# Performance work log

Measured on AMD Instinct MI355X. Metric: run time of the kernel, lower is better.

Reference implementation:

```python
import jax, jax.numpy as jnp
import numpy as np

ICM2IFS = 2.99792458e-05
KB = 0.6950389


def _forward(T, Er, cortim, dt, psi0, Hfull, W1, b1, W2, b2, W3, b3, W4, b4,
             save_interval, remat=False):
    # Faithful vectorized translation of MLNISE.forward with T_correction='ML',
    # explicitTemp='None', saveCoherence=False, saveU=False. The original
    # nested (ii, jj) Python loops are fully independent across (ii, jj), so
    # they are vectorized into one [B, N, N] pass per timestep.
    B, Tp1, N, _ = Hfull.shape
    kBT = T * KB                                             # [B]
    factor = (1j * 2.0 * np.pi * ICM2IFS) * dt.astype(jnp.complex64)  # [B]
    E0, C0 = jnp.linalg.eigh(Hfull[:, 0])
    phiB0 = jnp.einsum('bji,bjk->bik', C0.astype(jnp.complex64),
                       psi0.astype(jnp.complex64))           # Cold^T @ psi0
    jidx = jnp.arange(N)[None, :, None]

    def mlp(x):
        h = jax.nn.elu(x @ W1.T + b1)
        h = jax.nn.elu(h @ W2.T + b2)
        h = jax.nn.elu(h @ W3.T + b3)
        return jax.nn.elu(h @ W4.T + b4)

    def step(carry, Ht):
        Cold, Eold, phiB = carry
        E, C = jnp.linalg.eigh(Ht)
        S = jnp.einsum('bja,bjc->bac', C, Cold)              # S[b, jj, ii] = (C^T Cold)
        kk = jnp.argmax(S * S, axis=1)                       # [B, N] max over jj per ii
        is_kk = jidx == kk[:, None, :]                       # [B, N(jj), N(ii)]
        DE = jnp.where(is_kk, 0.0, E[:, :, None] - Eold[:, None, :])
        phi2 = jnp.real(phiB[:, :, 0]) ** 2 + jnp.imag(phiB[:, :, 0]) ** 2  # [B, N]
        p_ii = phi2[:, None, :]
        p_jj = phi2[:, :, None]
        m = p_ii > 0.01 * p_jj
        ratio = jnp.where(m, p_jj / jnp.where(m, p_ii, 1.0), 100.0)
        kbt = kBT[:, None, None]
        ones = jnp.ones_like(S)
        feat = jnp.stack([DE, ratio, S, kbt * ones,
                          Er[:, None, None] * ones, cortim[:, None, None] * ones,
                          jnp.zeros_like(S), jnp.exp(DE / kbt)], axis=-1)  # [B,N,N,8]
        corr = (mlp(feat.reshape(B * N * N, 8)) + 1.0).reshape(B, N, N)
        S2 = S * corr
        CD = jnp.sum(jnp.where(is_kk, 0.0, S2 * S2), axis=1)  # [B, N] per ii
        S_kk = jnp.take_along_axis(S2, kk[:, None, :], axis=1)[:, 0, :]  # [B, N]
        nrm = jnp.abs(S_kk)
        nrm = jnp.where(nrm > 0, nrm, 1.0)
        pos = (1.0 - CD) > 0
        newval = jnp.where(pos, jnp.sqrt(jnp.clip(1.0 - CD, 0.0)) * S_kk / nrm, S_kk)
        S2 = jnp.where(is_kk, newval[:, None, :], S2)
        phase = jnp.exp(-E.astype(jnp.complex64) * factor[:, None])  # [B, N]
        U = phase[:, :, None] * S2.astype(jnp.complex64)      # diag(phase) @ S
        phiB = U @ phiB
        phiB = phiB / jnp.sqrt(jnp.sum(jnp.real(phiB) ** 2 + jnp.imag(phiB) ** 2,
                                       axis=1, keepdims=True))
        ploc = jnp.einsum('bij,bjk->bik', C.astype(jnp.complex64), phiB)
        ps = jnp.real(ploc[:, :, 0]) ** 2 + jnp.imag(ploc[:, :, 0]) ** 2
        return (C, E, phiB), ps

    f = jax.checkpoint(step) if remat else step
    Hts = jnp.moveaxis(Hfull[:, 1:], 1, 0)                   # time-major [steps,B,N,N]
    _, ps_all = jax.lax.scan(f, (C0, E0, phiB0), Hts)
    saved = jnp.moveaxis(ps_all[save_interval - 1::save_interval], 0, 1)
    return jnp.concatenate([(psi0[:, :, 0] ** 2)[:, None, :], saved], axis=1)


def setup_inputs() -> dict:
    key = jax.random.key(0)
    ks = jax.random.split(key, 8)
    B, N, steps, SI = 32, 32, 600, 10
    A = 50.0 * jax.random.normal(ks[0], (B, steps + 1, N, N), dtype=jnp.float32)
    Hfull = 0.5 * (A + jnp.swapaxes(A, -1, -2))              # symmetric per snapshot
    psi0 = jnp.zeros((B, N, 1), jnp.float32).at[:, 0, 0].set(1.0)
    T = 250.0 + 100.0 * jax.random.uniform(ks[1], (B,), jnp.float32)
    Er = 1.0 + 35.0 * jax.random.uniform(ks[2], (B,), jnp.float32)
    cortim = 10.0 + 100.0 * jax.random.uniform(ks[3], (B,), jnp.float32)
    dt = jnp.ones((B,), jnp.float32)
    total_time = jnp.full((B,), float(steps), jnp.float32)
    reps = jnp.arange(B, dtype=jnp.int32)

    def lin(k, fo, fi):
        kw, kb = jax.random.split(k)
        bnd = 1.0 / np.sqrt(fi)
        W = jax.random.uniform(kw, (fo, fi), jnp.float32, -bnd, bnd) / 10.0
        b = jax.random.uniform(kb, (fo,), jnp.float32, -bnd, bnd)
        return W, b

    W1, b1 = lin(ks[4], 75, 8)
    W2, b2 = lin(ks[5], 75, 75)
    W3, b3 = lin(ks[6], 75, 75)
    W4, b4 = lin(ks[7], 1, 75)
    return dict(T=T, Er=Er, cortim=cortim, total_time=total_time, dt=dt, reps=reps,
                psi0=psi0, Hfull=Hfull, W1=W1, b1=b1, W2=W2, b2=b2, W3=W3, b3=b3,
                W4=W4, b4=b4, save_interval=SI)


def reference(T, Er, cortim, total_time, dt, reps, psi0, Hfull,
              W1, b1, W2, b2, W3, b3, W4, b4, save_interval):
    # total_time/dt only set the (static) number of steps = Hfull.shape[1]-1;
    # reps only sets the batch size. Both are encoded in the array shapes.
    return _forward(T, Er, cortim, dt, psi0, Hfull,
                    W1, b1, W2, b2, W3, b3, W4, b4, save_interval)
```

## Files before the change

### kernel.cpp

```cpp
#include <hip/hip_runtime.h>
#include <math.h>

#define NB 32
#define NN 32
#define NSTEPS 600
#define NT1 601
#define NSI 10
#define NH 75
#define NU 80
#define NKB 20
#define NIB 8

#define ICM2IFS 2.99792458e-05
#define KBOLTZ 0.6950389f
#define TWO_PI 6.283185307179586476925286766559

__device__ __forceinline__ float elu1(float x) { return x > 0.f ? x : (__expf(x) - 1.f); }

__global__ __launch_bounds__(64) void eigh_kernel(const float* __restrict__ Hf,
                                                  float* __restrict__ E_all,
                                                  float* __restrict__ CT_all)
{
    __shared__ double A[NN][NN + 1];
    __shared__ float  V[NN][NN + 1];
    __shared__ double csC[16], csS[16];
    __shared__ int   prC[16], qrC[16];
    __shared__ double redv;
    __shared__ int   rankl[NN];

    const int idx = blockIdx.x;
    const int tid = threadIdx.x;
    const float* Hp = Hf + (size_t)idx * (NN * NN);

    for (int e = tid; e < NN * NN; e += 64) {
        A[e >> 5][e & 31] = (double)Hp[e];
        V[e >> 5][e & 31] = ((e >> 5) == (e & 31)) ? 1.f : 0.f;
    }
    __syncthreads();

    double part = 0.0;
    for (int e = tid; e < NN * NN; e += 64) { double v = A[e >> 5][e & 31]; part += v * v; }
    #pragma unroll
    for (int off = 32; off > 0; off >>= 1) part += __shfl_down(part, off);
    if (tid == 0) redv = part;
    __syncthreads();
    const double tol2 = 1e-20 * redv;

    for (int sweep = 0; sweep < 10; ++sweep) {
        for (int r = 0; r < NN - 1; ++r) {
            if (tid < 16) {
                int m = tid, p, q;
                if (m == 0) { p = 0; q = 1 + (r % 31); }
                else { p = 1 + ((m + r) % 31); q = 1 + ((31 - m + r) % 31); }
                double apq = A[p][q];
                double c = 1.0, sn = 0.0;
                if (apq != 0.0) {
                    double theta = 0.5 * (A[q][q] - A[p][p]) / apq;
                    double tt = 1.0 / (fabs(theta) + sqrt(theta * theta + 1.0));
                    if (theta < 0.0) tt = -tt;
                    c = 1.0 / sqrt(tt * tt + 1.0);
                    sn = tt * c;
                }
                csC[m] = c; csS[m] = sn; prC[m] = p; qrC[m] = q;
            }
            __syncthreads();
            #pragma unroll
            for (int it = 0; it < 8; ++it) {
                int task = tid + it * 64;
                int m = task >> 5, jc = task & 31;
                int p = prC[m], q = qrC[m];
                double c = csC[m], sn = csS[m];
                double ap = A[p][jc], aq = A[q][jc];
                A[p][jc] = c * ap - sn * aq;
                A[q][jc] = sn * ap + c * aq;
            }
            __syncthreads();
            #pragma unroll
            for (int it = 0; it < 16; ++it) {
                int task = tid + it * 64;
                int m = (task >> 5) & 15, ir = task & 31;
                int p = prC[m], q = qrC[m];
                if (task < 512) {
                    double c = csC[m], sn = csS[m];
                    double aip = A[ir][p], aiq = A[ir][q];
                    A[ir][p] = c * aip - sn * aiq;
                    A[ir][q] = sn * aip + c * aiq;
                } else {
                    float cf = (float)csC[m], sf = (float)csS[m];
                    float vip = V[ir][p], viq = V[ir][q];
                    V[ir][p] = cf * vip - sf * viq;
                    V[ir][q] = sf * vip + cf * viq;
                }
            }
            __syncthreads();
        }
        if (sweep >= 3) {
            double o = 0.0;
            for (int e = tid; e < NN * NN; e += 64) {
                int i2 = e >> 5, j2 = e & 31;
                double v = A[i2][j2];
                o += (i2 != j2) ? v * v : 0.0;
            }
            #pragma unroll
            for (int off = 32; off > 0; off >>= 1) o += __shfl_down(o, off);
            if (tid == 0) redv = o;
            __syncthreads();
            if (redv <= tol2) break;
        }
    }
    __syncthreads();

    if (tid < NN) {
        double ei = A[tid][tid];
        int rk = 0;
        for (int j2 = 0; j2 < NN; ++j2) {
            double ej = A[j2][j2];
            rk += (ej < ei || (ej == ei && j2 < tid)) ? 1 : 0;
        }
        rankl[tid] = rk;
        E_all[(size_t)idx * NN + rk] = (float)ei;
    }
    __syncthreads();
    float* ct = CT_all + (size_t)idx * NN * NN;
    for (int e = tid; e < NN * NN; e += 64) {
        int col = e >> 5, m2 = e & 31;
        ct[(size_t)rankl[col] * NN + m2] = V[m2][col];
    }
}

__global__ __launch_bounds__(256) void kk_kernel(const float* __restrict__ CT_all,
                                                 int* __restrict__ kk_all)
{
    __shared__ float Ct[NN][NN + 1], Cp[NN][NN + 1], S[NN][NN + 1];
    const int blk = blockIdx.x;
    const int b = blk / NSTEPS, s = blk % NSTEPS + 1;
    const int tid = threadIdx.x;
    const float* ctg = CT_all + ((size_t)b * NT1 + s) * (NN * NN);
    const float* cpg = CT_all + ((size_t)b * NT1 + s - 1) * (NN * NN);
    for (int e = tid; e < NN * NN; e += 256) {
        Ct[e >> 5][e & 31] = ctg[e];
        Cp[e >> 5][e & 31] = cpg[e];
    }
    __syncthreads();
    for (int e = tid; e < NN * NN; e += 256) {
        int i = e >> 5, j = e & 31;
        float acc = 0.f;
        for (int m = 0; m < NN; ++m) acc += Ct[i][m] * Cp[j][m];
        S[i][j] = acc;
    }
    __syncthreads();
    if (tid < NN) {
        const int j = tid;
        float best = -1.f; int bi = 0;
        for (int i = 0; i < NN; ++i) {
            float v = S[i][j]; v *= v;
            if (v > best) { best = v; bi = i; }
        }
        kk_all[(size_t)blk * NN + j] = bi;
    }
}

__global__ void wtrans_kernel(const float* __restrict__ W1, const float* __restrict__ b1,
                              const float* __restrict__ W2, const float* __restrict__ W3,
                              const float* __restrict__ b2, const float* __restrict__ b3,
                              const float* __restrict__ W4,
                              float* __restrict__ W2p, float* __restrict__ W3p,
                              float4* __restrict__ L1W4, float4* __restrict__ L1B4,
                              float* __restrict__ bpad)
{
    const int tid = threadIdx.x;
    const int tot = 8 * NKB * 4 * 12;
    for (int e = tid; e < tot; e += 256) {
        int ug = e / (NKB * 4 * 12);
        int kb = (e / (4 * 12)) % NKB;
        int kp = (e / 12) & 3;
        int uu = e % 12;
        int u = ug * 10 + uu;
        int k = kb * 4 + kp;
        float v2 = 0.f, v3 = 0.f;
        if (uu < 10 && u < NH && k < NH) {
            v2 = W2[u * NH + k];
            v3 = W3[u * NH + k];
        }
        W2p[e] = v2; W3p[e] = v3;
    }
    if (tid < NU) {
        if (tid < NH) {
            const float* w = W1 + tid * 8;
            L1W4[tid] = make_float4(w[0], w[1], w[2], w[7]);
            L1B4[tid] = make_float4(w[3], w[4], w[5], b1[tid]);
            bpad[tid]          = b2[tid];
            bpad[NU + tid]     = b3[tid];
            bpad[2 * NU + tid] = W4[tid];
        } else {
            L1W4[tid] = make_float4(0.f, 0.f, 0.f, 0.f);
            L1B4[tid] = make_float4(0.f, 0.f, 0.f, 0.f);
            bpad[tid] = 0.f; bpad[NU + tid] = 0.f; bpad[2 * NU + tid] = 0.f;
        }
    }
}

__global__ __launch_bounds__(512, 2) void persist_kernel(
    const float* __restrict__ E_all, const float* __restrict__ CT_all,
    const int* __restrict__ kk_all, const float* __restrict__ psi0,
    const float* __restrict__ Tarr, const float* __restrict__ ErA,
    const float* __restrict__ ctA, const float* __restrict__ dtA,
    const float* __restrict__ W2p, const float* __restrict__ W3p,
    const float4* __restrict__ L1W4g, const float4* __restrict__ L1B4g,
    const float* __restrict__ bpad, const float* __restrict__ b4v,
    float* __restrict__ S2T_g, unsigned int* __restrict__ cnt,
    float* __restrict__ out)
{
    extern __shared__ __align__(16) float dyn[];
    float4* L1Wl = (float4*)dyn;
    float4* L1Bl = L1Wl + NU;
    float* cst  = (float*)(L1Bl + NU);
    float* b2l  = cst + NU;
    float* b3l  = b2l + NU;
    float* W4l  = b3l + NU;
    float* hbuf = W4l + NU;
    float (*S2T)[NN + 4] = (float(*)[NN + 4])hbuf;

    __shared__ float CpN[2][NN][NN + 4];
    __shared__ float4 featS[128];
    __shared__ float2 a4b2[8][64];
    __shared__ float EL[2][NN];
    __shared__ int   kkL[2][NN];
    __shared__ double phre[NN], phim[NN], redl[NN], nreS[NN], nimS[NN];
    __shared__ float phi2l[NN];

    const int tid  = threadIdx.x;
    const int b    = blockIdx.x >> 3;
    const int iblk = blockIdx.x & 7;
    const int j0   = iblk * 4;
    const int ug   = __builtin_amdgcn_readfirstlane(tid >> 6);
    const int rg   = tid & 63;
    const int U    = ug * 10;

    const float kbt = KBOLTZ * Tarr[b];
    const float er  = ErA[b];
    const float cti = ctA[b];
    const double dtb = (double)dtA[b];
    const float b4s = b4v[0];

    const float4* W2g = (const float4*)(W2p + (size_t)ug * (NKB * 48));
    const float4* W3g = (const float4*)(W3p + (size_t)ug * (NKB * 48));

    if (tid < NU) {
        L1Wl[tid] = L1W4g[tid];
        L1Bl[tid] = L1B4g[tid];
        b2l[tid] = bpad[tid];
        b3l[tid] = bpad[NU + tid];
        W4l[tid] = bpad[2 * NU + tid];
    }
    __syncthreads();
    if (tid < NU) {
        float4 lb = L1Bl[tid];
        cst[tid] = lb.w + lb.x * kbt + lb.y * er + lb.z * cti;
    }

    {
        const float* c0g = CT_all + (size_t)b * NT1 * NN * NN;
        const float* c1g = c0g + NN * NN;
        for (int e = tid; e < NN * NN; e += 512) {
            CpN[0][e >> 5][e & 31] = c0g[e];
            CpN[1][e >> 5][e & 31] = c1g[e];
        }
        if (tid < NN) {
            EL[0][tid] = E_all[((size_t)b * NT1 + 0) * NN + tid];
            EL[1][tid] = E_all[((size_t)b * NT1 + 1) * NN + tid];
            kkL[1][tid] = kk_all[(size_t)b * NSTEPS * NN + tid];
        }
        __syncthreads();
        if (tid < NN) {
            const int i = tid;
            double acc = 0.0;
            for (int j = 0; j < NN; ++j) acc += (double)CpN[0][i][j] * (double)psi0[b * NN + j];
            phre[i] = acc; phim[i] = 0.0;
            phi2l[i] = (float)(acc * acc);
            if (iblk == 0) {
                float p0 = psi0[b * NN + i];
                out[((size_t)b * 61) * NN + i] = p0 * p0;
            }
        }
        __syncthreads();
        {
            const int r = tid >> 2, c = tid & 3;
            const int i = r & 31, j = j0 + (r >> 5);
            float Sv = 0.f;
            #pragma unroll
            for (int m = c; m < NN; m += 4)
                Sv += CpN[1][i][m] * CpN[0][j][m];
            Sv += __shfl_xor(Sv, 1); Sv += __shfl_xor(Sv, 2);
            if (c == 0) {
                const int kj = kkL[1][j];
                const float DE = (i == kj) ? 0.f : (EL[1][i] - EL[0][j]);
                featS[r] = make_float4(DE, 100.f, Sv, __expf(DE / kbt));
            }
        }
        __syncthreads();
        if (tid < 128) {
            const int i = tid & 31, j = j0 + (tid >> 5);
            const float p_i = phi2l[i], p_j = phi2l[j];
            featS[tid].y = (p_j > 0.01f * p_i) ? (p_i / p_j) : 100.f;
        }
    }

    for (int t = 1; t <= NSTEPS; ++t) {
        __syncthreads();
        const int cur = t & 1;

        float2 cpre = make_float2(0.f, 0.f);
        float  epre = 0.f;
        int    kpre = 0;
        if (t < NSTEPS) {
            const float* c1g = CT_all + ((size_t)b * NT1 + t + 1) * (NN * NN);
            cpre = ((const float2*)c1g)[tid];
            if (tid < NN) epre = E_all[((size_t)b * NT1 + t + 1) * NN + tid];
            else if (tid < 2 * NN) kpre = kk_all[((size_t)b * NSTEPS + t) * NN + (tid - NN)];
        }

        {
            float4 f0 = featS[2 * rg], f1 = featS[2 * rg + 1];
            #pragma unroll
            for (int u = 0; u < 10; ++u) {
                float4 wv = L1Wl[U + u];
                float c = cst[U + u];
                float2 hv;
                hv.x = elu1(c + wv.x * f0.x + wv.y * f0.y + wv.z * f0.z + wv.w * f0.w);
                hv.y = elu1(c + wv.x * f1.x + wv.y * f1.y + wv.z * f1.z + wv.w * f1.w);
                *(float2*)(hbuf + (U + u) * 128 + 2 * rg) = hv;
            }
        }
        __syncthreads();

        float2 acc[10];
        #pragma unroll
        for (int u = 0; u < 10; ++u) { float bb = b2l[U + u]; acc[u] = make_float2(bb, bb); }
        for (int kb = 0; kb < NKB; ++kb) {
            float4 wv[12];
            float2 hv[4];
            #pragma unroll
            for (int m = 0; m < 12; ++m) wv[m] = W2g[kb * 12 + m];
            #pragma unroll
            for (int kk = 0; kk < 4; ++kk)
                hv[kk] = *(const float2*)(hbuf + (kb * 4 + kk) * 128 + 2 * rg);
            #pragma unroll
            for (int kk = 0; kk < 4; ++kk) {
                const float* wf = (const float*)&wv[kk * 3];
                #pragma unroll
                for (int u = 0; u < 10; ++u) {
                    float wS = wf[u];
                    acc[u].x += wS * hv[kk].x; acc[u].y += wS * hv[kk].y;
                }
            }
        }
        __syncthreads();
        #pragma unroll
        for (int u = 0; u < 10; ++u) {
            float2 hv; hv.x = elu1(acc[u].x); hv.y = elu1(acc[u].y);
            *(float2*)(hbuf + (U + u) * 128 + 2 * rg) = hv;
        }
        __syncthreads();

        #pragma unroll
        for (int u = 0; u < 10; ++u) { float bb = b3l[U + u]; acc[u] = make_float2(bb, bb); }
        for (int kb = 0; kb < NKB; ++kb) {
            float4 wv[12];
            float2 hv[4];
            #pragma unroll
            for (int m = 0; m < 12; ++m) wv[m] = W3g[kb * 12 + m];
            #pragma unroll
            for (int kk = 0; kk < 4; ++kk)
                hv[kk] = *(const float2*)(hbuf + (kb * 4 + kk) * 128 + 2 * rg);
            #pragma unroll
            for (int kk = 0; kk < 4; ++kk) {
                const float* wf = (const float*)&wv[kk * 3];
                #pragma unroll
                for (int u = 0; u < 10; ++u) {
                    float wS = wf[u];
                    acc[u].x += wS * hv[kk].x; acc[u].y += wS * hv[kk].y;
                }
            }
        }
        {
            float2 p4 = make_float2(0.f, 0.f);
            #pragma unroll
            for (int u = 0; u < 10; ++u) {
                float w4 = W4l[U + u];
                p4.x += w4 * elu1(acc[u].x); p4.y += w4 * elu1(acc[u].y);
            }
            a4b2[ug][rg] = p4;
        }
        __syncthreads();

        if (tid < 128) {
            const int r = tid;
            const int i = r & 31;
            const int j = j0 + (r >> 5);
            float a4 = b4s;
            #pragma unroll
            for (int g = 0; g < 8; ++g) {
                float2 pv = a4b2[g][r >> 1];
                a4 += (r & 1) ? pv.y : pv.x;
            }
            const float corr = elu1(a4) + 1.f;
            float s2v = featS[r].z * corr;
            const int kj = kkL[cur][j];
            double v = (double)s2v;
            double cd = (i == kj) ? 0.0 : v * v;
            cd += __shfl_xor(cd, 1);  cd += __shfl_xor(cd, 2);
            cd += __shfl_xor(cd, 4);  cd += __shfl_xor(cd, 8);
            cd += __shfl_xor(cd, 16);
            if (i == kj) {
                double nrm = fabs(v); nrm = (nrm > 0.0) ? nrm : 1.0;
                double rem = 1.0 - cd;
                s2v = (float)((rem > 0.0) ? (sqrt(rem) * v / nrm) : v);
            }
            __hip_atomic_store(&S2T_g[(((size_t)cur * NB + b) * NN + j) * NN + i],
                               s2v, __ATOMIC_RELAXED, __HIP_MEMORY_SCOPE_AGENT);
            asm volatile("s_waitcnt vmcnt(0)" ::: "memory");
            if ((tid & 63) == 0)
                __hip_atomic_fetch_add(cnt + (size_t)b * NSTEPS + (t - 1), 1u,
                                       __ATOMIC_RELAXED, __HIP_MEMORY_SCOPE_AGENT);
        }

        if (t < NSTEPS) {
            const int e0 = tid * 2;
            CpN[1 - cur][e0 >> 5][e0 & 31] = cpre.x;
            CpN[1 - cur][e0 >> 5][(e0 & 31) + 1] = cpre.y;
            if (tid < NN) EL[1 - cur][tid] = epre;
            else if (tid < 2 * NN) kkL[1 - cur][tid - NN] = kpre;
        }
        __syncthreads();

        if (t < NSTEPS) {
            const int curS = 1 - cur;
            const int r = tid >> 2, c = tid & 3;
            const int i = r & 31, j = j0 + (r >> 5);
            float Sv = 0.f;
            #pragma unroll
            for (int m = c; m < NN; m += 4)
                Sv += CpN[curS][i][m] * CpN[1 - curS][j][m];
            Sv += __shfl_xor(Sv, 1); Sv += __shfl_xor(Sv, 2);
            if (c == 0) {
                const int kj = kkL[curS][j];
                const float DE = (i == kj) ? 0.f : (EL[curS][i] - EL[1 - curS][j]);
                featS[r] = make_float4(DE, 100.f, Sv, __expf(DE / kbt));
            }
        }

        if (tid == 0) {
            const unsigned int* c = cnt + (size_t)b * NSTEPS + (t - 1);
            while (__hip_atomic_load(c, __ATOMIC_RELAXED, __HIP_MEMORY_SCOPE_AGENT)
                   < 2u * NIB) {
                __builtin_amdgcn_s_sleep(4);
            }
        }
        __syncthreads();

        {
            const unsigned long long* s2u = (const unsigned long long*)
                (S2T_g + ((size_t)cur * NB + b) * (NN * NN));
            for (int e = tid; e < (NN * NN) / 2; e += 512) {
                unsigned long long w = __hip_atomic_load(&s2u[e], __ATOMIC_RELAXED,
                                                         __HIP_MEMORY_SCOPE_AGENT);
                float2 f = *(float2*)&w;
                const int e0 = e * 2;
                S2T[e0 >> 5][e0 & 31] = f.x;
                S2T[e0 >> 5][(e0 & 31) + 1] = f.y;
            }
        }
        __syncthreads();

        {
            const int ii = tid >> 4, l = tid & 15;
            double are = 0.0, aim = 0.0;
            #pragma unroll
            for (int jj = l; jj < NN; jj += 16) {
                double sv = (double)S2T[jj][ii];
                are += sv * phre[jj]; aim += sv * phim[jj];
            }
            are += __shfl_xor(are, 1); aim += __shfl_xor(aim, 1);
            are += __shfl_xor(are, 2); aim += __shfl_xor(aim, 2);
            are += __shfl_xor(are, 4); aim += __shfl_xor(aim, 4);
            are += __shfl_xor(are, 8); aim += __shfl_xor(aim, 8);
            if (l == 0) {
                double th = (double)EL[cur][ii] * (TWO_PI * ICM2IFS) * dtb;
                double x2 = th * th;
                double sph = th * (1.0 + x2 * (-1.0 / 6.0 + x2 * (1.0 / 120.0 + x2 * (-1.0 / 5040.0 + x2 * (1.0 / 362880.0)))));
                double cph = 1.0 + x2 * (-0.5 + x2 * (1.0 / 24.0 + x2 * (-1.0 / 720.0 + x2 * (1.0 / 40320.0))));
                double nre = cph * are + sph * aim;
                double nim = cph * aim - sph * are;
                nreS[ii] = nre; nimS[ii] = nim;
                redl[ii] = nre * nre + nim * nim;
            }
        }
        __syncthreads();

        if (tid < NN) {
            double v = redl[tid];
            v += __shfl_xor(v, 1); v += __shfl_xor(v, 2); v += __shfl_xor(v, 4);
            v += __shfl_xor(v, 8); v += __shfl_xor(v, 16);
            double sc = 1.0 / sqrt(v);
            double nr = nreS[tid] * sc, ni = nimS[tid] * sc;
            phre[tid] = nr; phim[tid] = ni;
            phi2l[tid] = (float)(nr * nr + ni * ni);
        }
        __syncthreads();

        if ((t % NSI) == 0 && tid < 64) {
            const int ii = iblk * 4 + (tid >> 4), l = tid & 15;
            double are = 0.0, aim = 0.0;
            #pragma unroll
            for (int jj = l; jj < NN; jj += 16) {
                double cij = (double)CpN[cur][jj][ii];
                are += cij * phre[jj]; aim += cij * phim[jj];
            }
            are += __shfl_xor(are, 1); aim += __shfl_xor(aim, 1);
            are += __shfl_xor(are, 2); aim += __shfl_xor(aim, 2);
            are += __shfl_xor(are, 4); aim += __shfl_xor(aim, 4);
            are += __shfl_xor(are, 8); aim += __shfl_xor(aim, 8);
            if (l == 0)
                out[((size_t)b * 61 + t / NSI) * NN + ii] = (float)(are * are + aim * aim);
        }
        if (t < NSTEPS && tid < 128) {
            const int i = tid & 31, j = j0 + (tid >> 5);
            const float p_i = phi2l[i], p_j = phi2l[j];
            featS[tid].y = (p_j > 0.01f * p_i) ? (p_i / p_j) : 100.f;
        }
    }
}

extern "C" void kernel_launch(void* const* d_in, const int* in_sizes, int n_in,
                              void* d_out, int out_size, void* d_ws, size_t ws_size,
                              hipStream_t stream)
{
    const float* Tarr = (const float*)d_in[0];
    const float* ErA  = (const float*)d_in[1];
    const float* ctA  = (const float*)d_in[2];
    const float* dtA  = (const float*)d_in[4];
    const float* psi0 = (const float*)d_in[6];
    const float* Hf   = (const float*)d_in[7];
    const float* W1   = (const float*)d_in[8];
    const float* b1   = (const float*)d_in[9];
    const float* W2   = (const float*)d_in[10];
    const float* b2   = (const float*)d_in[11];
    const float* W3   = (const float*)d_in[12];
    const float* b3   = (const float*)d_in[13];
    const float* W4   = (const float*)d_in[14];
    const float* b4   = (const float*)d_in[15];

    unsigned int* cnt = (unsigned int*)d_ws;
    float* E_all  = (float*)(cnt + (size_t)NB * NSTEPS);
    float* CT_all = E_all + (size_t)NB * NT1 * NN;
    float* W2p    = CT_all + (size_t)NB * NT1 * NN * NN;
    float* W3p    = W2p + 8 * NKB * 48;
    float4* L1W4  = (float4*)(W3p + 8 * NKB * 48);
    float4* L1B4  = L1W4 + NU;
    float* bpad   = (float*)(L1B4 + NU);
    float* S2T_g  = bpad + 3 * NU;
    int*   kk_all = (int*)(S2T_g + 2 * (size_t)NB * NN * NN);
    float* outp   = (float*)d_out;

    hipMemsetAsync(cnt, 0, (size_t)NB * NSTEPS * sizeof(unsigned int), stream);
    eigh_kernel<<<NB * NT1, 64, 0, stream>>>(Hf, E_all, CT_all);
    wtrans_kernel<<<1, 256, 0, stream>>>(W1, b1, W2, W3, b2, b3, W4,
                                         W2p, W3p, L1W4, L1B4, bpad);
    kk_kernel<<<NB * NSTEPS, 256, 0, stream>>>(CT_all, kk_all);

    const size_t dynf = (size_t)(8 * NU) + 4 * NU + NU * 128;
    persist_kernel<<<NB * NIB, 512, dynf * sizeof(float), stream>>>(E_all, CT_all,
        kk_all, psi0, Tarr, ErA, ctA, dtA, W2p, W3p, L1W4, L1B4, bpad, b4,
        S2T_g, cnt, outp);
}
```

Baseline: 14.65 ms.

## Exchange per-block partial psi products instead of full S2 matrix across blocks

```diff
diff --git a/kernel.cpp b/kernel.cpp
--- a/kernel.cpp
+++ b/kernel.cpp
@@ -1,5 +1,6 @@
 #include <hip/hip_runtime.h>
 #include <math.h>
+
 
 #define NB 32
 #define NN 32
@@ -17,9 +18,9 @@
 
 __device__ __forceinline__ float elu1(float x) { return x > 0.f ? x : (__expf(x) - 1.f); }
 
-__global__ __launch_bounds__(64) void eigh_kernel(const float* __restrict__ Hf,
-                                                  float* __restrict__ E_all,
-                                                  float* __restrict__ CT_all)
+__global__ __launch_bounds__(128) void eigh_kernel(const float* __restrict__ Hf,
+                                                   float* __restrict__ E_all,
+                                                   float* __restrict__ CT_all)
 {
     __shared__ double A[NN][NN + 1];
     __shared__ float  V[NN][NN + 1];
@@ -32,17 +33,19 @@
     const int tid = threadIdx.x;
     const float* Hp = Hf + (size_t)idx * (NN * NN);
 
-    for (int e = tid; e < NN * NN; e += 64) {
+    for (int e = tid; e < NN * NN; e += 128) {
         A[e >> 5][e & 31] = (double)Hp[e];
         V[e >> 5][e & 31] = ((e >> 5) == (e & 31)) ? 1.f : 0.f;
     }
     __syncthreads();
 
-    double part = 0.0;
-    for (int e = tid; e < NN * NN; e += 64) { double v = A[e >> 5][e & 31]; part += v * v; }
-    #pragma unroll
-    for (int off = 32; off > 0; off >>= 1) part += __shfl_down(part, off);
-    if (tid == 0) redv = part;
+    if (tid < 64) {
+        double part = 0.0;
+        for (int e = tid; e < NN * NN; e += 64) { double v = A[e >> 5][e & 31]; part += v * v; }
+        #pragma unroll
+        for (int off = 32; off > 0; off >>= 1) part += __shfl_down(part, off);
+        if (tid == 0) redv = part;
+    }
     __syncthreads();
     const double tol2 = 1e-20 * redv;
 
@@ -65,8 +68,8 @@
             }
             __syncthreads();
             #pragma unroll
-            for (int it = 0; it < 8; ++it) {
-                int task = tid + it * 64;
+            for (int it = 0; it < 4; ++it) {
+                int task = tid + it * 128;
                 int m = task >> 5, jc = task & 31;
                 int p = prC[m], q = qrC[m];
                 double c = csC[m], sn = csS[m];
@@ -76,8 +79,8 @@
             }
             __syncthreads();
             #pragma unroll
-            for (int it = 0; it < 16; ++it) {
-                int task = tid + it * 64;
+            for (int it = 0; it < 8; ++it) {
+                int task = tid + it * 128;
                 int m = (task >> 5) & 15, ir = task & 31;
                 int p = prC[m], q = qrC[m];
                 if (task < 512) {
@@ -95,15 +98,17 @@
             __syncthreads();
         }
         if (sweep >= 3) {
-            double o = 0.0;
-            for (int e = tid; e < NN * NN; e += 64) {
-                int i2 = e >> 5, j2 = e & 31;
-                double v = A[i2][j2];
-                o += (i2 != j2) ? v * v : 0.0;
-            }
-            #pragma unroll
-            for (int off = 32; off > 0; off >>= 1) o += __shfl_down(o, off);
-            if (tid == 0) redv = o;
+            if (tid < 64) {
+                double o = 0.0;
+                for (int e = tid; e < NN * NN; e += 64) {
+                    int i2 = e >> 5, j2 = e & 31;
+                    double v = A[i2][j2];
+                    o += (i2 != j2) ? v * v : 0.0;
+                }
+                #pragma unroll
+                for (int off = 32; off > 0; off >>= 1) o += __shfl_down(o, off);
+                if (tid == 0) redv = o;
+            }
             __syncthreads();
             if (redv <= tol2) break;
         }
@@ -122,7 +127,7 @@
     }
     __syncthreads();
     float* ct = CT_all + (size_t)idx * NN * NN;
-    for (int e = tid; e < NN * NN; e += 64) {
+    for (int e = tid; e < NN * NN; e += 128) {
         int col = e >> 5, m2 = e & 31;
         ct[(size_t)rankl[col] * NN + m2] = V[m2][col];
     }
@@ -208,7 +213,7 @@
     const float* __restrict__ W2p, const float* __restrict__ W3p,
     const float4* __restrict__ L1W4g, const float4* __restrict__ L1B4g,
     const float* __restrict__ bpad, const float* __restrict__ b4v,
-    float* __restrict__ S2T_g, unsigned int* __restrict__ cnt,
+    double* __restrict__ part_g, unsigned int* __restrict__ cnt,
     float* __restrict__ out)
 {
     extern __shared__ __align__(16) float dyn[];
@@ -219,14 +224,15 @@
     float* b3l  = b2l + NU;
     float* W4l  = b3l + NU;
     float* hbuf = W4l + NU;
-    float (*S2T)[NN + 4] = (float(*)[NN + 4])hbuf;
 
     __shared__ float CpN[2][NN][NN + 4];
     __shared__ float4 featS[128];
     __shared__ float2 a4b2[8][64];
     __shared__ float EL[2][NN];
     __shared__ int   kkL[2][NN];
-    __shared__ double phre[NN], phim[NN], redl[NN], nreS[NN], nimS[NN];
+    __shared__ double phre[NN], phim[NN];
+    __shared__ double ppre[4][NN], ppim[4][NN];
+    __shared__ double sre[NN], sim[NN];
     __shared__ float phi2l[NN];
 
     const int tid  = threadIdx.x;
@@ -397,7 +403,8 @@
         if (tid < 128) {
             const int r = tid;
             const int i = r & 31;
-            const int j = j0 + (r >> 5);
+            const int jj = r >> 5;
+            const int j = j0 + jj;
             float a4 = b4s;
             #pragma unroll
             for (int g = 0; g < 8; ++g) {
@@ -415,14 +422,11 @@
             if (i == kj) {
                 double nrm = fabs(v); nrm = (nrm > 0.0) ? nrm : 1.0;
                 double rem = 1.0 - cd;
-                s2v = (float)((rem > 0.0) ? (sqrt(rem) * v / nrm) : v);
-            }
-            __hip_atomic_store(&S2T_g[(((size_t)cur * NB + b) * NN + j) * NN + i],
-                               s2v, __ATOMIC_RELAXED, __HIP_MEMORY_SCOPE_AGENT);
-            asm volatile("s_waitcnt vmcnt(0)" ::: "memory");
-            if ((tid & 63) == 0)
-                __hip_atomic_fetch_add(cnt + (size_t)b * NSTEPS + (t - 1), 1u,
-                                       __ATOMIC_RELAXED, __HIP_MEMORY_SCOPE_AGENT);
+                v = (rem > 0.0) ? (sqrt(rem) * v / nrm) : v;
+                v = (double)(float)v;
+            }
+            ppre[jj][i] = v * phre[j];
+            ppim[jj][i] = v * phim[j];
         }
 
         if (t < NSTEPS) {
@@ -433,6 +437,21 @@
             else if (tid < 2 * NN) kkL[1 - cur][tid - NN] = kpre;
         }
         __syncthreads();
+
+        if (tid < 32) {
+            const int i = tid;
+            double pr = ((ppre[0][i] + ppre[1][i]) + ppre[2][i]) + ppre[3][i];
+            double pi = ((ppim[0][i] + ppim[1][i]) + ppim[2][i]) + ppim[3][i];
+            double* pg = part_g + ((size_t)cur * NB + b) * 512;
+            __hip_atomic_store(&pg[i * 8 + iblk], pr,
+                               __ATOMIC_RELAXED, __HIP_MEMORY_SCOPE_AGENT);
+            __hip_atomic_store(&pg[256 + i * 8 + iblk], pi,
+                               __ATOMIC_RELAXED, __HIP_MEMORY_SCOPE_AGENT);
+            asm volatile("s_waitcnt vmcnt(0)" ::: "memory");
+            if (tid == 0)
+                __hip_atomic_fetch_add(cnt + (size_t)b * NSTEPS + (t - 1), 1u,
+                                       __ATOMIC_RELAXED, __HIP_MEMORY_SCOPE_AGENT);
+        }
 
         if (t < NSTEPS) {
             const int curS = 1 - cur;
@@ -453,59 +472,41 @@
         if (tid == 0) {
             const unsigned int* c = cnt + (size_t)b * NSTEPS + (t - 1);
             while (__hip_atomic_load(c, __ATOMIC_RELAXED, __HIP_MEMORY_SCOPE_AGENT)
-                   < 2u * NIB) {
-                __builtin_amdgcn_s_sleep(4);
+                   < (unsigned)NIB) {
+                __builtin_amdgcn_s_sleep(2);
             }
         }
         __syncthreads();
 
         {
-            const unsigned long long* s2u = (const unsigned long long*)
-                (S2T_g + ((size_t)cur * NB + b) * (NN * NN));
-            for (int e = tid; e < (NN * NN) / 2; e += 512) {
-                unsigned long long w = __hip_atomic_load(&s2u[e], __ATOMIC_RELAXED,
-                                                         __HIP_MEMORY_SCOPE_AGENT);
-                float2 f = *(float2*)&w;
-                const int e0 = e * 2;
-                S2T[e0 >> 5][e0 & 31] = f.x;
-                S2T[e0 >> 5][(e0 & 31) + 1] = f.y;
-            }
-        }
-        __syncthreads();
-
-        {
-            const int ii = tid >> 4, l = tid & 15;
-            double are = 0.0, aim = 0.0;
-            #pragma unroll
-            for (int jj = l; jj < NN; jj += 16) {
-                double sv = (double)S2T[jj][ii];
-                are += sv * phre[jj]; aim += sv * phim[jj];
-            }
-            are += __shfl_xor(are, 1); aim += __shfl_xor(aim, 1);
-            are += __shfl_xor(are, 2); aim += __shfl_xor(aim, 2);
-            are += __shfl_xor(are, 4); aim += __shfl_xor(aim, 4);
-            are += __shfl_xor(are, 8); aim += __shfl_xor(aim, 8);
-            if (l == 0) {
-                double th = (double)EL[cur][ii] * (TWO_PI * ICM2IFS) * dtb;
-                double x2 = th * th;
-                double sph = th * (1.0 + x2 * (-1.0 / 6.0 + x2 * (1.0 / 120.0 + x2 * (-1.0 / 5040.0 + x2 * (1.0 / 362880.0)))));
-                double cph = 1.0 + x2 * (-0.5 + x2 * (1.0 / 24.0 + x2 * (-1.0 / 720.0 + x2 * (1.0 / 40320.0))));
-                double nre = cph * are + sph * aim;
-                double nim = cph * aim - sph * are;
-                nreS[ii] = nre; nimS[ii] = nim;
-                redl[ii] = nre * nre + nim * nim;
+            const double* pg = part_g + ((size_t)cur * NB + b) * 512;
+            double v = __hip_atomic_load(&pg[tid], __ATOMIC_RELAXED,
+                                         __HIP_MEMORY_SCOPE_AGENT);
+            v += __shfl_xor(v, 1); v += __shfl_xor(v, 2); v += __shfl_xor(v, 4);
+            if ((tid & 7) == 0) {
+                const int i = (tid >> 3) & 31;
+                if (tid < 256) sre[i] = v; else sim[i] = v;
             }
         }
         __syncthreads();
 
         if (tid < NN) {
-            double v = redl[tid];
-            v += __shfl_xor(v, 1); v += __shfl_xor(v, 2); v += __shfl_xor(v, 4);
-            v += __shfl_xor(v, 8); v += __shfl_xor(v, 16);
-            double sc = 1.0 / sqrt(v);
-            double nr = nreS[tid] * sc, ni = nimS[tid] * sc;
-            phre[tid] = nr; phim[tid] = ni;
-            phi2l[tid] = (float)(nr * nr + ni * ni);
+            const int ii = tid;
+            double are = sre[ii], aim = sim[ii];
+            double th = (double)EL[cur][ii] * (TWO_PI * ICM2IFS) * dtb;
+            double x2 = th * th;
+            double sph = th * (1.0 + x2 * (-1.0 / 6.0 + x2 * (1.0 / 120.0 + x2 * (-1.0 / 5040.0 + x2 * (1.0 / 362880.0)))));
+            double cph = 1.0 + x2 * (-0.5 + x2 * (1.0 / 24.0 + x2 * (-1.0 / 720.0 + x2 * (1.0 / 40320.0))));
+            double nre = cph * are + sph * aim;
+            double nim = cph * aim - sph * are;
+            double v = nre * nre + nim * nim;
+            double s = v;
+            s += __shfl_xor(s, 1); s += __shfl_xor(s, 2); s += __shfl_xor(s, 4);
+            s += __shfl_xor(s, 8); s += __shfl_xor(s, 16);
+            double sc = 1.0 / sqrt(s);
+            double nr = nre * sc, ni = nim * sc;
+            phre[ii] = nr; phim[ii] = ni;
+            phi2l[ii] = (float)(nr * nr + ni * ni);
         }
         __syncthreads();
 
@@ -559,12 +560,12 @@
     float4* L1W4  = (float4*)(W3p + 8 * NKB * 48);
     float4* L1B4  = L1W4 + NU;
     float* bpad   = (float*)(L1B4 + NU);
-    float* S2T_g  = bpad + 3 * NU;
-    int*   kk_all = (int*)(S2T_g + 2 * (size_t)NB * NN * NN);
+    double* part_g = (double*)(bpad + 3 * NU);
+    int*   kk_all = (int*)(part_g + 2 * (size_t)NB * 512);
     float* outp   = (float*)d_out;
 
     hipMemsetAsync(cnt, 0, (size_t)NB * NSTEPS * sizeof(unsigned int), stream);
-    eigh_kernel<<<NB * NT1, 64, 0, stream>>>(Hf, E_all, CT_all);
+    eigh_kernel<<<NB * NT1, 128, 0, stream>>>(Hf, E_all, CT_all);
     wtrans_kernel<<<1, 256, 0, stream>>>(W1, b1, W2, W3, b2, b3, W4,
                                          W2p, W3p, L1W4, L1B4, bpad);
     kk_kernel<<<NB * NSTEPS, 256, 0, stream>>>(CT_all, kk_all);
@@ -572,5 +573,5 @@
     const size_t dynf = (size_t)(8 * NU) + 4 * NU + NU * 128;
     persist_kernel<<<NB * NIB, 512, dynf * sizeof(float), stream>>>(E_all, CT_all,
         kk_all, psi0, Tarr, ErA, ctA, dtA, W2p, W3p, L1W4, L1B4, bpad, b4,
-        S2T_g, cnt, outp);
+        part_g, cnt, outp);
 }
```

New measurement: 13.70 ms. -6.4%, faster.
